# Kernel optimization log

Measured on AMD Instinct MI355X. Metric: run time of the kernel, lower is better.

Reference implementation:

```python
import jax, jax.numpy as jnp
import numpy as np
import math

B, T, C, H, L, V = 4, 2048, 256, 4, 2, 1024
HS = C // H  # head size


def setup_inputs() -> dict:
    key = jax.random.key(0)
    ks = jax.random.split(key, 10)
    s = 0.02
    return {
        "tokens": jax.random.randint(ks[0], (B, T), 0, V),
        "wte": s * jax.random.normal(ks[1], (V + 1, C), dtype=jnp.float32),
        "ln1_g": jnp.ones((L, C), jnp.float32),
        "ln1_b": jnp.zeros((L, C), jnp.float32),
        "attn_w": s * jax.random.normal(ks[2], (L, 3 * C, C), dtype=jnp.float32),
        "attn_b": jnp.zeros((L, 3 * C), jnp.float32),
        "proj_w": s * jax.random.normal(ks[3], (L, C, C), dtype=jnp.float32),
        "proj_b": jnp.zeros((L, C), jnp.float32),
        "embk": s * jax.random.normal(ks[4], (L, T, HS), dtype=jnp.float32),
        "embv": s * jax.random.normal(ks[5], (L, T, HS), dtype=jnp.float32),
        "ln2_g": jnp.ones((L, C), jnp.float32),
        "ln2_b": jnp.zeros((L, C), jnp.float32),
        "fc_w": s * jax.random.normal(ks[6], (L, 4 * C, C), dtype=jnp.float32),
        "fc_b": jnp.zeros((L, 4 * C), jnp.float32),
        "mproj_w": s * jax.random.normal(ks[7], (L, C, 4 * C), dtype=jnp.float32),
        "mproj_b": jnp.zeros((L, C), jnp.float32),
        "lnf_g": jnp.ones((C,), jnp.float32),
        "lnf_b": jnp.zeros((C,), jnp.float32),
        "head_w": s * jax.random.normal(ks[8], (V, C), dtype=jnp.float32),
    }


def _ln(x, g, b):
    mu = x.mean(-1, keepdims=True)
    var = x.var(-1, keepdims=True)
    return (x - mu) / jnp.sqrt(var + 1e-5) * g + b


def _gelu(x):  # NewGELU (tanh approximation)
    return 0.5 * x * (1.0 + jnp.tanh(math.sqrt(2.0 / math.pi) * (x + 0.044715 * x ** 3)))


def reference(tokens, wte, ln1_g, ln1_b, attn_w, attn_b, proj_w, proj_b,
              embk, embv, ln2_g, ln2_b, fc_w, fc_b, mproj_w, mproj_b,
              lnf_g, lnf_b, head_w):
    x = wte[tokens]  # [B,T,C]; no absolute pos emb in this model
    idx = jnp.arange(T)
    rel = jnp.tril(idx[:, None] - idx[None, :])  # [T,T] nonneg offsets
    causal = idx[:, None] >= idx[None, :]
    scale = 1.0 / math.sqrt(HS)
    for l in range(L):
        h = _ln(x, ln1_g[l], ln1_b[l])
        qkv = h @ attn_w[l].T + attn_b[l]  # [B,T,3C]
        q, k, v = jnp.split(qkv, 3, axis=-1)
        q = q.reshape(B, T, H, HS).transpose(0, 2, 1, 3)  # [B,H,T,hs]
        k = k.reshape(B, T, H, HS).transpose(0, 2, 1, 3)
        v = v.reshape(B, T, H, HS).transpose(0, 2, 1, 3)
        rk = embk[l][rel]  # [T,T,hs]
        rv = embv[l][rel]  # [T,T,hs]
        att = jnp.einsum('bhtd,bhsd->bhts', q, k) * scale \
            + jnp.einsum('bhtd,tsd->bhts', q, rk)
        att = jnp.where(causal, att, -jnp.inf)
        att = jax.nn.softmax(att, axis=-1)
        y = jnp.einsum('bhts,bhsd->bhtd', att, v) \
            + jnp.einsum('bhts,tsd->bhtd', att, rv)
        y = y.transpose(0, 2, 1, 3).reshape(B, T, C)
        x = x + (y @ proj_w[l].T + proj_b[l])
        h2 = _ln(x, ln2_g[l], ln2_b[l])
        x = x + (_gelu(h2 @ fc_w[l].T + fc_b[l]) @ mproj_w[l].T + mproj_b[l])
    x = _ln(x, lnf_g, lnf_b)
    return x @ head_w.T  # [B,T,V] logits
```

## Files before the change

### kernel.cpp

```cpp
#include <hip/hip_runtime.h>
#include <hip/hip_bf16.h>
#include <math.h>

#define BB 4
#define TT 2048
#define CC 256
#define HH 4
#define LL 2
#define VV 1024
#define HS 64
#define EPAD 2176
#define LOG2E 1.4426950408889634f

typedef __attribute__((ext_vector_type(8))) __bf16 bf16x8;
typedef __attribute__((ext_vector_type(4))) float f32x4;

#define MFMA16(a, b, c) __builtin_amdgcn_mfma_f32_16x16x32_bf16((a), (b), (c), 0, 0, 0)

__device__ __forceinline__ ushort f2bf(float f) {
    __hip_bfloat16 h = __float2bfloat16(f);
    return *reinterpret_cast<ushort*>(&h);
}
__device__ __forceinline__ float bf2f(ushort u) {
    union { uint i; float f; } c; c.i = ((uint)u) << 16; return c.f;
}

__device__ __forceinline__ void gload16(const void* g, void* l) {
    __builtin_amdgcn_global_load_lds(
        (const __attribute__((address_space(1))) void*)g,
        (__attribute__((address_space(3))) void*)l, 16, 0, 0);
}

__device__ __forceinline__ float gelu_f(float v) {
    return 0.5f * v * (1.0f + tanhf(0.7978845608028654f * (v + 0.044715f * v * v * v)));
}

__global__ void embed_kernel(const int* __restrict__ tok,
                             const float* __restrict__ wte,
                             float* __restrict__ x) {
    int row = blockIdx.x;
    int tid = threadIdx.x;
    int tk = tok[row];
    x[(size_t)row * CC + tid] = wte[(size_t)tk * CC + tid];
}

__global__ void cvt5_kernel(const float* __restrict__ w0, const float* __restrict__ w1,
                            const float* __restrict__ w2, const float* __restrict__ w3,
                            const float* __restrict__ w4,
                            ushort* __restrict__ o0, ushort* __restrict__ o1,
                            ushort* __restrict__ o2, ushort* __restrict__ o3,
                            ushort* __restrict__ o4) {
    int i = blockIdx.x * 256 + threadIdx.x;
    const float* src; ushort* dst; int j;
    if (i < 98304)       { src = w0; dst = o0; j = i; }
    else if (i < 131072) { src = w1; dst = o1; j = i - 98304; }
    else if (i < 262144) { src = w2; dst = o2; j = i - 131072; }
    else if (i < 393216) { src = w3; dst = o3; j = i - 262144; }
    else                 { src = w4; dst = o4; j = i - 393216; }
    float4 v = ((const float4*)src)[j];
    ushort4 o;
    o.x = f2bf(v.x); o.y = f2bf(v.y); o.z = f2bf(v.z); o.w = f2bf(v.w);
    ((ushort4*)dst)[j] = o;
}

__global__ __launch_bounds__(256) void ln_kernel(const float* __restrict__ x,
                                                 const float* __restrict__ g,
                                                 const float* __restrict__ b,
                                                 ushort* __restrict__ out) {
    int row = blockIdx.x * 4 + (threadIdx.x >> 6);
    int lane = threadIdx.x & 63;
    float4 v = ((const float4*)(x + (size_t)row * CC))[lane];
    float s = v.x + v.y + v.z + v.w;
    float s2 = v.x * v.x + v.y * v.y + v.z * v.z + v.w * v.w;
    for (int m = 1; m < 64; m <<= 1) {
        s += __shfl_xor(s, m);
        s2 += __shfl_xor(s2, m);
    }
    float mean = s * (1.0f / CC);
    float var = s2 * (1.0f / CC) - mean * mean;
    float rs = rsqrtf(var + 1e-5f);
    float4 gg = ((const float4*)g)[lane];
    float4 bb = ((const float4*)b)[lane];
    ushort4 o;
    o.x = f2bf((v.x - mean) * rs * gg.x + bb.x);
    o.y = f2bf((v.y - mean) * rs * gg.y + bb.y);
    o.z = f2bf((v.z - mean) * rs * gg.z + bb.z);
    o.w = f2bf((v.w - mean) * rs * gg.w + bb.w);
    ((ushort4*)(out + (size_t)row * CC))[lane] = o;
}

template<int MODE>
__global__ __launch_bounds__(256) void bgemm128_kernel(
        const ushort* __restrict__ A, const ushort* __restrict__ W,
        const float* __restrict__ bias, float* __restrict__ out,
        ushort* __restrict__ outb, int N, int K,
        ushort* __restrict__ qb, ushort* __restrict__ kb,
        ushort* __restrict__ vtb) {
    constexpr int ASUB = 8, TOT = 12, BUFSH = 192 * 32;
    __shared__ ushort lds[2 * BUFSH];
    int tid = threadIdx.x;
    int w = tid >> 6, lane = tid & 63;
    int lo = lane & 15, hi = lane >> 4;
    int row0 = blockIdx.y * 128;
    int col0 = blockIdx.x * 64;
    int wm = w >> 1, wn = w & 1;
    const ushort* Asrc = A + (size_t)row0 * K;
    const ushort* Wsrc = W + (size_t)col0 * K;

    auto STAGE = [&](int buf, int k0) {
        ushort* dst = &lds[buf * BUFSH];
        for (int s = w; s < TOT; s += 4) {
            const ushort* src;
            if (s < ASUB) src = Asrc + (size_t)(s * 16 + lo) * K + k0 + hi * 8;
            else          src = Wsrc + (size_t)((s - ASUB) * 16 + lo) * K + k0 + hi * 8;
            gload16(src, dst + s * 512);
        }
    };

    f32x4 acc[4][2] = {};
    int NT = K >> 5;
    STAGE(0, 0);
    asm volatile("s_waitcnt vmcnt(0)" ::: "memory");
    __syncthreads();
    for (int t = 0; t < NT; ++t) {
        int buf = t & 1;
        if (t + 1 < NT) STAGE(buf ^ 1, (t + 1) << 5);
        bf16x8 a[4], b[2];
#pragma unroll
        for (int f = 0; f < 4; ++f)
            a[f] = *(const bf16x8*)&lds[buf * BUFSH + (wm * 4 + f) * 512 + lane * 8];
#pragma unroll
        for (int g = 0; g < 2; ++g)
            b[g] = *(const bf16x8*)&lds[buf * BUFSH + (ASUB + wn * 2 + g) * 512 + lane * 8];
        __builtin_amdgcn_s_setprio(1);
#pragma unroll
        for (int f = 0; f < 4; ++f)
#pragma unroll
            for (int g = 0; g < 2; ++g)
                acc[f][g] = MFMA16(a[f], b[g], acc[f][g]);
        __builtin_amdgcn_s_setprio(0);
        asm volatile("s_waitcnt vmcnt(0)" ::: "memory");
        __syncthreads();
    }
#pragma unroll
    for (int f = 0; f < 4; ++f) {
        int rr = row0 + wm * 64 + f * 16 + hi * 4;
#pragma unroll
        for (int g = 0; g < 2; ++g) {
            int cc = col0 + wn * 32 + g * 16 + lo;
            float bv = bias ? bias[cc] : 0.0f;
#pragma unroll
            for (int j = 0; j < 4; ++j) {
                int r = rr + j;
                float v = acc[f][g][j] + bv;
                if (MODE == 3) {
                    int t = r & 2047, bb2 = r >> 11;
                    int which = cc >> 8, hh = (cc >> 6) & 3, dd = cc & 63;
                    size_t bh = (size_t)(bb2 * 4 + hh);
                    if (which == 0)      qb[(bh * 2048 + t) * 64 + dd] = f2bf(v);
                    else if (which == 1) kb[(bh * 2048 + t) * 64 + dd] = f2bf(v * (0.125f * LOG2E));
                    else                 vtb[(bh * 64 + dd) * 2048 + t] = f2bf(v);
                } else if (MODE == 2) {
                    outb[(size_t)r * N + cc] = f2bf(gelu_f(v));
                } else {
                    out[(size_t)r * N + cc] = v;
                }
            }
        }
    }
}

__global__ __launch_bounds__(256) void bgemm64_kernel(
        const ushort* __restrict__ A, const ushort* __restrict__ W,
        const float* __restrict__ bias, float* __restrict__ out,
        int N, int K) {
    constexpr int ASUB = 8, TOT = 16, BUFSH = 128 * 64;
    __shared__ ushort lds[2 * BUFSH];
    int tid = threadIdx.x;
    int w = tid >> 6, lane = tid & 63;
    int lo = lane & 15, hi = lane >> 4;
    int row0 = blockIdx.y * 64;
    int col0 = blockIdx.x * 64;
    const ushort* Asrc = A + (size_t)row0 * K;
    const ushort* Wsrc = W + (size_t)col0 * K;

    auto STAGE = [&](int buf, int k0) {
        ushort* dst = &lds[buf * BUFSH];
        for (int s = w; s < TOT; s += 4) {
            const ushort* src;
            if (s < ASUB) {
                int rg = s >> 1, kh = s & 1;
                src = Asrc + (size_t)(rg * 16 + lo) * K + k0 + kh * 32 + hi * 8;
            } else {
                int s2 = s - ASUB;
                int cg = s2 >> 1, kh = s2 & 1;
                src = Wsrc + (size_t)(cg * 16 + lo) * K + k0 + kh * 32 + hi * 8;
            }
            gload16(src, dst + s * 512);
        }
    };

    f32x4 acc[4] = {};
    int NT = K >> 6;
    STAGE(0, 0);
    asm volatile("s_waitcnt vmcnt(0)" ::: "memory");
    __syncthreads();
    for (int t = 0; t < NT; ++t) {
        int buf = t & 1;
        if (t + 1 < NT) STAGE(buf ^ 1, (t + 1) << 6);
        bf16x8 a[2];
#pragma unroll
        for (int kh = 0; kh < 2; ++kh)
            a[kh] = *(const bf16x8*)&lds[buf * BUFSH + (w * 2 + kh) * 512 + lane * 8];
        __builtin_amdgcn_s_setprio(1);
#pragma unroll
        for (int g = 0; g < 4; ++g) {
#pragma unroll
            for (int kh = 0; kh < 2; ++kh) {
                bf16x8 b = *(const bf16x8*)&lds[buf * BUFSH + (ASUB + g * 2 + kh) * 512 + lane * 8];
                acc[g] = MFMA16(a[kh], b, acc[g]);
            }
        }
        __builtin_amdgcn_s_setprio(0);
        asm volatile("s_waitcnt vmcnt(0)" ::: "memory");
        __syncthreads();
    }
#pragma unroll
    for (int g = 0; g < 4; ++g) {
        int cc = col0 + g * 16 + lo;
        float bv = bias ? bias[cc] : 0.0f;
#pragma unroll
        for (int j = 0; j < 4; ++j) {
            int r = row0 + w * 16 + hi * 4 + j;
            out[(size_t)r * N + cc] += acc[g][j] + bv;
        }
    }
}

__global__ void emb_bf_kernel(const float* __restrict__ ek,
                              const float* __restrict__ ev,
                              ushort* __restrict__ ekp,
                              ushort* __restrict__ evtp) {
    int i = blockIdx.x * 256 + threadIdx.x;
    int rp = i >> 6, d = i & 63;
    int o = rp - 64;
    bool in = (o >= 0 && o < TT);
    float kv = in ? ek[(size_t)o * 64 + d] * LOG2E : 0.0f;
    float vv = in ? ev[(size_t)o * 64 + d] : 0.0f;
    ekp[(size_t)rp * 64 + d] = f2bf(kv);
    evtp[(size_t)d * EPAD + rp] = f2bf(vv);
}

#define SBUF 57344
#define KOFF 0
#define VOFF 8192
#define EKOFF 16384
#define EVOFF 32768
#define WSCR (2 * SBUF)

__global__ __launch_bounds__(512, 2) void flash_kernel(
        const ushort* __restrict__ qb,
        const ushort* __restrict__ kb,
        const ushort* __restrict__ vtb,
        const ushort* __restrict__ ekp,
        const ushort* __restrict__ evtp,
        ushort* __restrict__ y) {
    extern __shared__ __align__(16) char dls[];

    int g = blockIdx.x;
    int lbid = ((g & 7) << 5) | (g >> 3);
    int bh = lbid >> 4;
    int pk = lbid & 15;
    int tid = threadIdx.x;
    int w = tid >> 6;
    int sub = w & 3;
    int h = w >> 2;
    int lane = tid & 63;
    int lo = lane & 15, hi = lane >> 4;
    int sw = (lo & 7) << 4;

    char* wbase = dls + WSCR + w * 6144;
    ushort (*Rl)[88]   = (ushort (*)[88])  wbase;
    ushort (*Pl)[72]   = (ushort (*)[72])  wbase;
    ushort (*Ppl)[104] = (ushort (*)[104])(wbase + 2816);

    {
        uint* pz = reinterpret_cast<uint*>(&Ppl[0][0]);
        for (int i = lane; i < 832; i += 64) pz[i] = 0;
    }

    const char* kB  = (const char*)(kb  + (size_t)bh * 2048 * 64);
    const char* vB  = (const char*)(vtb + (size_t)bh * 64 * 2048);
    const char* ekB = (const char*)ekp;
    const char* evB = (const char*)evtp;

    int t0A = (31 - pk) * 64, t0B = pk * 64;
    int NSA = 32 - pk;
    const int NC = 33;

    auto STAGE = [&](int buf, int ci) {
        int t0 = (ci < NSA) ? t0A : t0B;
        int s0 = ((ci < NSA) ? ci : ci - NSA) * 64;
        int band0 = t0 - s0;
        char* B = dls + buf * SBUF;
        int wb = (tid & 448) << 4;
        {
            int gb = tid * 16;
            int r = gb >> 7, c = gb & 127;
            gload16(kB + (size_t)(s0 + r) * 128 + (c ^ ((r & 7) << 4)), B + KOFF + wb);
        }
        {
            int gb = tid * 16;
            int r = gb >> 7, c = gb & 127;
            gload16(vB + (size_t)r * 4096 + (size_t)s0 * 2 + (c ^ ((r & 7) << 4)),
                    B + VOFF + wb);
        }
#pragma unroll
        for (int p = 0; p < 2; ++p) {
            int gb = p * 8192 + tid * 16;
            int r = gb >> 7, c = gb & 127;
            gload16(ekB + (size_t)(band0 + r) * 128 + (c ^ ((r & 7) << 4)),
                    B + EKOFF + p * 8192 + wb);
        }
#pragma unroll
        for (int p = 0; p < 3; ++p) {
            int gb = p * 8192 + tid * 16;
            int r = gb / 384, c = gb - r * 384;
            gload16(evB + (size_t)r * 4352 + (size_t)band0 * 2 + (c ^ ((r & 7) << 4)),
                    B + EVOFF + p * 8192 + wb);
        }
    };

    STAGE(0, 0);
    asm volatile("s_waitcnt vmcnt(0)" ::: "memory");
    __syncthreads();

    int b_ = bh >> 2, h_ = bh & 3;
    int buf = 0, ci = 0;
    int nb = h ? 0 : 2;
    int kcA = h ? 0 : 1, kcB = h ? 1 : 2;

    for (int tile = 0; tile < 2; ++tile) {
        int t0 = tile ? t0B : t0A;
        int NS = tile ? (pk + 1) : NSA;

        const ushort* qbase = qb + ((size_t)bh * 2048 + t0 + sub * 16) * 64;
        bf16x8 qf0 = *(const bf16x8*)(qbase + (size_t)lo * 64 + hi * 8);
        bf16x8 qf1 = *(const bf16x8*)(qbase + (size_t)lo * 64 + 32 + hi * 8);

        float rs[4] = {0.0f, 0.0f, 0.0f, 0.0f};
        f32x4 O[4] = {};

        for (int c = 0; c < NS; ++c, ++ci) {
            if (ci + 1 < NC) STAGE(buf ^ 1, ci + 1);
            const char* B = dls + buf * SBUF;
            bool diag = (c == NS - 1);

            f32x4 sacc[2] = {};
            __builtin_amdgcn_s_setprio(1);
#pragma unroll
            for (int ni = 0; ni < 2; ++ni) {
                int R = (2 * h + ni) * 16 + lo;
                bf16x8 b0 = *(const bf16x8*)(B + KOFF + R * 128 + ((hi * 16) ^ sw));
                bf16x8 b1 = *(const bf16x8*)(B + KOFF + R * 128 + ((64 + hi * 16) ^ sw));
                sacc[ni] = MFMA16(qf0, b0, sacc[ni]);
                sacc[ni] = MFMA16(qf1, b1, sacc[ni]);
            }
#pragma unroll
            for (int ni = 0; ni < 3; ++ni) {
                int n = nb + ni;
                int RL = (sub + n) * 16 + lo;
                f32x4 r = {};
                bf16x8 e0 = *(const bf16x8*)(B + EKOFF + RL * 128 + ((hi * 16) ^ sw));
                bf16x8 e1 = *(const bf16x8*)(B + EKOFF + RL * 128 + ((64 + hi * 16) ^ sw));
                r = MFMA16(qf0, e0, r);
                r = MFMA16(qf1, e1, r);
#pragma unroll
                for (int j = 0; j < 4; ++j) Rl[hi * 4 + j][n * 16 + lo] = f2bf(r[j]);
            }
            __builtin_amdgcn_s_setprio(0);
            float sv[2][4];
#pragma unroll
            for (int ni = 0; ni < 2; ++ni) {
                int sl = (2 * h + ni) * 16 + lo;
#pragma unroll
                for (int j = 0; j < 4; ++j) {
                    int r_ = hi * 4 + j;
                    sv[ni][j] = sacc[ni][j] + bf2f(Rl[r_][r_ - sl + 64]);
                }
            }
            asm volatile("" ::: "memory");
#pragma unroll
            for (int ni = 0; ni < 2; ++ni) {
                int sl = (2 * h + ni) * 16 + lo;
#pragma unroll
                for (int j = 0; j < 4; ++j) {
                    int r_ = hi * 4 + j;
                    float p = (!diag || sl <= sub * 16 + r_) ? exp2f(sv[ni][j]) : 0.0f;
                    rs[j] += p;
                    ushort pu = f2bf(p);
                    Pl[r_][sl] = pu;
                    Ppl[r_][r_ - sl + 64] = pu;
                }
            }
            asm volatile("" ::: "memory");

            __builtin_amdgcn_s_setprio(1);
            bf16x8 pa  = *(const bf16x8*)(&Pl[lo][h * 32 + hi * 8]);
            bf16x8 pb0 = *(const bf16x8*)(&Ppl[lo][kcA * 32 + hi * 8]);
            bf16x8 pb1 = *(const bf16x8*)(&Ppl[lo][kcB * 32 + hi * 8]);
#pragma unroll
            for (int n = 0; n < 4; ++n) {
                int R = n * 16 + lo;
                bf16x8 bv = *(const bf16x8*)(B + VOFF + R * 128 + ((h * 64 + hi * 16) ^ sw));
                O[n] = MFMA16(pa, bv, O[n]);
                bf16x8 e0 = *(const bf16x8*)(B + EVOFF + R * 384 +
                                             ((sub * 32 + kcA * 64 + hi * 16) ^ sw));
                O[n] = MFMA16(pb0, e0, O[n]);
                bf16x8 e1 = *(const bf16x8*)(B + EVOFF + R * 384 +
                                             ((sub * 32 + kcB * 64 + hi * 16) ^ sw));
                O[n] = MFMA16(pb1, e1, O[n]);
            }
            __builtin_amdgcn_s_setprio(0);
            asm volatile("" ::: "memory");

            asm volatile("s_waitcnt vmcnt(0)" ::: "memory");
            __syncthreads();
            buf ^= 1;
        }

#pragma unroll
        for (int msk = 1; msk < 16; msk <<= 1)
#pragma unroll
            for (int j = 0; j < 4; ++j) rs[j] += __shfl_xor(rs[j], msk);

        char* mscr = dls + (buf ^ 1) * SBUF + sub * 8192;
        if (h == 1) {
            float* Of = (float*)mscr;
#pragma unroll
            for (int n = 0; n < 4; ++n)
#pragma unroll
                for (int j = 0; j < 4; ++j)
                    Of[(hi * 4 + j) * 64 + n * 16 + lo] = O[n][j];
            if (lo == 0)
#pragma unroll
                for (int j = 0; j < 4; ++j)
                    ((float*)(mscr + 4096))[hi * 4 + j] = rs[j];
        }
        __syncthreads();
        if (h == 0) {
            float* Of = (float*)mscr;
            float inv[4];
#pragma unroll
            for (int j = 0; j < 4; ++j)
                inv[j] = 1.0f / (rs[j] + ((float*)(mscr + 4096))[hi * 4 + j]);
#pragma unroll
            for (int n = 0; n < 4; ++n)
#pragma unroll
                for (int j = 0; j < 4; ++j) {
                    int r = t0 + sub * 16 + hi * 4 + j;
                    float v = O[n][j] + Of[(hi * 4 + j) * 64 + n * 16 + lo];
                    y[((size_t)(b_ * 2048 + r)) * 256 + h_ * 64 + n * 16 + lo] =
                        f2bf(v * inv[j]);
                }
        }
        __syncthreads();
    }
}

extern "C" void kernel_launch(void* const* d_in, const int* in_sizes, int n_in,
                              void* d_out, int out_size, void* d_ws, size_t ws_size,
                              hipStream_t stream) {
    const int*   tokens  = (const int*)d_in[0];
    const float* wte     = (const float*)d_in[1];
    const float* ln1_g   = (const float*)d_in[2];
    const float* ln1_b   = (const float*)d_in[3];
    const float* attn_w  = (const float*)d_in[4];
    const float* attn_b  = (const float*)d_in[5];
    const float* proj_w  = (const float*)d_in[6];
    const float* proj_b  = (const float*)d_in[7];
    const float* embk    = (const float*)d_in[8];
    const float* embv    = (const float*)d_in[9];
    const float* ln2_g   = (const float*)d_in[10];
    const float* ln2_b   = (const float*)d_in[11];
    const float* fc_w    = (const float*)d_in[12];
    const float* fc_b    = (const float*)d_in[13];
    const float* mproj_w = (const float*)d_in[14];
    const float* mproj_b = (const float*)d_in[15];
    const float* lnf_g   = (const float*)d_in[16];
    const float* lnf_b   = (const float*)d_in[17];
    const float* head_w  = (const float*)d_in[18];
    float* out = (float*)d_out;

    const int M = BB * TT;
    char* wsb = (char*)d_ws;
    float*  x    = (float*)wsb;
    ushort* h    = (ushort*)(wsb + ((size_t)8 << 20));
    ushort* y    = (ushort*)(wsb + ((size_t)12 << 20));
    ushort* qb   = (ushort*)(wsb + ((size_t)16 << 20));
    ushort* kbf  = (ushort*)(wsb + ((size_t)20 << 20));
    ushort* vtb  = (ushort*)(wsb + ((size_t)24 << 20));
    ushort* ekp  = (ushort*)(wsb + ((size_t)28 << 20));
    ushort* evtp = (ushort*)(wsb + ((size_t)28 << 20) + 524288);
    ushort* attn_wb  = (ushort*)(wsb + ((size_t)29 << 20));
    ushort* proj_wb  = attn_wb + (size_t)LL * 3 * CC * CC;
    ushort* fc_wb    = proj_wb + (size_t)LL * CC * CC;
    ushort* mproj_wb = fc_wb + (size_t)LL * 4 * CC * CC;
    ushort* head_wb  = mproj_wb + (size_t)LL * CC * 4 * CC;
    ushort* fcb = (ushort*)d_out;

    dim3 blk(256);
    const int FLDS = WSCR + 8 * 6144;
    hipFuncSetAttribute(reinterpret_cast<const void*>(flash_kernel),
                        hipFuncAttributeMaxDynamicSharedMemorySize, FLDS);

    cvt5_kernel<<<dim3(1792), blk, 0, stream>>>(
        attn_w, proj_w, fc_w, mproj_w, head_w,
        attn_wb, proj_wb, fc_wb, mproj_wb, head_wb);

    embed_kernel<<<dim3(M), blk, 0, stream>>>(tokens, wte, x);

    for (int l = 0; l < LL; l++) {
        ln_kernel<<<dim3(M / 4), blk, 0, stream>>>(x, ln1_g + l * CC, ln1_b + l * CC, h);
        bgemm128_kernel<3><<<dim3(12, 64), blk, 0, stream>>>(
            h, attn_wb + (size_t)l * 3 * CC * CC, attn_b + (size_t)l * 3 * CC,
            nullptr, nullptr, 3 * CC, CC, qb, kbf, vtb);
        emb_bf_kernel<<<dim3(EPAD * 64 / 256), blk, 0, stream>>>(
            embk + (size_t)l * TT * HS, embv + (size_t)l * TT * HS, ekp, evtp);
        flash_kernel<<<dim3(256), dim3(512), FLDS, stream>>>(qb, kbf, vtb, ekp, evtp, y);
        bgemm64_kernel<<<dim3(4, 128), blk, 0, stream>>>(
            y, proj_wb + (size_t)l * CC * CC, proj_b + (size_t)l * CC,
            x, CC, CC);
        ln_kernel<<<dim3(M / 4), blk, 0, stream>>>(x, ln2_g + l * CC, ln2_b + l * CC, h);
        bgemm128_kernel<2><<<dim3(16, 64), blk, 0, stream>>>(
            h, fc_wb + (size_t)l * 4 * CC * CC, fc_b + (size_t)l * 4 * CC,
            nullptr, fcb, 4 * CC, CC, nullptr, nullptr, nullptr);
        bgemm64_kernel<<<dim3(4, 128), blk, 0, stream>>>(
            fcb, mproj_wb + (size_t)l * CC * 4 * CC, mproj_b + (size_t)l * CC,
            x, CC, 4 * CC);
    }

    ln_kernel<<<dim3(M / 4), blk, 0, stream>>>(x, lnf_g, lnf_b, h);
    bgemm128_kernel<0><<<dim3(16, 64), blk, 0, stream>>>(
        h, head_wb, nullptr, out, nullptr, VV, CC, nullptr, nullptr, nullptr);
}
```

Baseline: 335.5 us.

## Load full K=256 tiles into LDS once and widen K=1024 GEMM tiles

For the K=256 GEMMs, the new kernel loads the whole 128x256 A tile and 64x256 W tile into dynamic LDS in a single burst. It then runs eight MFMA k-steps with no per-step barrier or double buffering. The proj and mproj GEMMs (previously 64-row tiles, K chunks of 64) now use 128x64 tiles with K chunks of 128 and a 4x2 accumulator per warp. The aim is to cut barriers and raise reuse per load, at the cost of 96KB LDS per block, which lowers occupancy, and halved grid sizes for the N=256 GEMMs.

```diff
diff --git a/kernel.cpp b/kernel.cpp
--- a/kernel.cpp
+++ b/kernel.cpp
@@ -90,58 +90,55 @@
 }
 
 template<int MODE>
-__global__ __launch_bounds__(256) void bgemm128_kernel(
+__global__ __launch_bounds__(256) void bgfull_kernel(
         const ushort* __restrict__ A, const ushort* __restrict__ W,
         const float* __restrict__ bias, float* __restrict__ out,
-        ushort* __restrict__ outb, int N, int K,
+        ushort* __restrict__ outb, int N,
         ushort* __restrict__ qb, ushort* __restrict__ kb,
         ushort* __restrict__ vtb) {
-    constexpr int ASUB = 8, TOT = 12, BUFSH = 192 * 32;
-    __shared__ ushort lds[2 * BUFSH];
+    extern __shared__ ushort flds[];
+    const int K = 256;
     int tid = threadIdx.x;
     int w = tid >> 6, lane = tid & 63;
     int lo = lane & 15, hi = lane >> 4;
     int row0 = blockIdx.y * 128;
     int col0 = blockIdx.x * 64;
     int wm = w >> 1, wn = w & 1;
-    const ushort* Asrc = A + (size_t)row0 * K;
-    const ushort* Wsrc = W + (size_t)col0 * K;
-
-    auto STAGE = [&](int buf, int k0) {
-        ushort* dst = &lds[buf * BUFSH];
-        for (int s = w; s < TOT; s += 4) {
-            const ushort* src;
-            if (s < ASUB) src = Asrc + (size_t)(s * 16 + lo) * K + k0 + hi * 8;
-            else          src = Wsrc + (size_t)((s - ASUB) * 16 + lo) * K + k0 + hi * 8;
-            gload16(src, dst + s * 512);
-        }
-    };
-
-    f32x4 acc[4][2] = {};
-    int NT = K >> 5;
-    STAGE(0, 0);
+
+#pragma unroll
+    for (int i = 0; i < 24; ++i) {
+        int s = w * 24 + i;
+        if (s < 64) {
+            int rg = s >> 3, kg = s & 7;
+            gload16(A + (size_t)(row0 + rg * 16 + lo) * K + kg * 32 + hi * 8,
+                    &flds[s * 512]);
+        } else {
+            int s2 = s - 64;
+            int cg = s2 >> 3, kg = s2 & 7;
+            gload16(W + (size_t)(col0 + cg * 16 + lo) * K + kg * 32 + hi * 8,
+                    &flds[32768 + s2 * 512]);
+        }
+    }
     asm volatile("s_waitcnt vmcnt(0)" ::: "memory");
     __syncthreads();
-    for (int t = 0; t < NT; ++t) {
-        int buf = t & 1;
-        if (t + 1 < NT) STAGE(buf ^ 1, (t + 1) << 5);
+
+    f32x4 acc[4][2] = {};
+#pragma unroll
+    for (int kg = 0; kg < 8; ++kg) {
         bf16x8 a[4], b[2];
 #pragma unroll
         for (int f = 0; f < 4; ++f)
-            a[f] = *(const bf16x8*)&lds[buf * BUFSH + (wm * 4 + f) * 512 + lane * 8];
+            a[f] = *(const bf16x8*)&flds[((wm * 4 + f) * 8 + kg) * 512 + lane * 8];
 #pragma unroll
         for (int g = 0; g < 2; ++g)
-            b[g] = *(const bf16x8*)&lds[buf * BUFSH + (ASUB + wn * 2 + g) * 512 + lane * 8];
-        __builtin_amdgcn_s_setprio(1);
+            b[g] = *(const bf16x8*)&flds[32768 + ((wn * 2 + g) * 8 + kg) * 512 + lane * 8];
 #pragma unroll
         for (int f = 0; f < 4; ++f)
 #pragma unroll
             for (int g = 0; g < 2; ++g)
                 acc[f][g] = MFMA16(a[f], b[g], acc[f][g]);
-        __builtin_amdgcn_s_setprio(0);
-        asm volatile("s_waitcnt vmcnt(0)" ::: "memory");
-        __syncthreads();
-    }
+    }
+
 #pragma unroll
     for (int f = 0; f < 4; ++f) {
         int rr = row0 + wm * 64 + f * 16 + hi * 4;
@@ -162,6 +159,8 @@
                     else                 vtb[(bh * 64 + dd) * 2048 + t] = f2bf(v);
                 } else if (MODE == 2) {
                     outb[(size_t)r * N + cc] = f2bf(gelu_f(v));
+                } else if (MODE == 1) {
+                    out[(size_t)r * N + cc] += v;
                 } else {
                     out[(size_t)r * N + cc] = v;
                 }
@@ -170,69 +169,71 @@
     }
 }
 
-__global__ __launch_bounds__(256) void bgemm64_kernel(
+__global__ __launch_bounds__(256) void bgk1024_kernel(
         const ushort* __restrict__ A, const ushort* __restrict__ W,
-        const float* __restrict__ bias, float* __restrict__ out,
-        int N, int K) {
-    constexpr int ASUB = 8, TOT = 16, BUFSH = 128 * 64;
-    __shared__ ushort lds[2 * BUFSH];
+        const float* __restrict__ bias, float* __restrict__ out, int N) {
+    extern __shared__ ushort flds[];
+    const int K = 1024;
+    constexpr int BUF = 24576;
     int tid = threadIdx.x;
     int w = tid >> 6, lane = tid & 63;
     int lo = lane & 15, hi = lane >> 4;
-    int row0 = blockIdx.y * 64;
+    int row0 = blockIdx.y * 128;
     int col0 = blockIdx.x * 64;
-    const ushort* Asrc = A + (size_t)row0 * K;
-    const ushort* Wsrc = W + (size_t)col0 * K;
+    int wm = w >> 1, wn = w & 1;
 
     auto STAGE = [&](int buf, int k0) {
-        ushort* dst = &lds[buf * BUFSH];
-        for (int s = w; s < TOT; s += 4) {
-            const ushort* src;
-            if (s < ASUB) {
-                int rg = s >> 1, kh = s & 1;
-                src = Asrc + (size_t)(rg * 16 + lo) * K + k0 + kh * 32 + hi * 8;
+#pragma unroll
+        for (int i = 0; i < 12; ++i) {
+            int s = w * 12 + i;
+            if (s < 32) {
+                int rg = s >> 2, kg = s & 3;
+                gload16(A + (size_t)(row0 + rg * 16 + lo) * K + k0 + kg * 32 + hi * 8,
+                        &flds[buf * BUF + s * 512]);
             } else {
-                int s2 = s - ASUB;
-                int cg = s2 >> 1, kh = s2 & 1;
-                src = Wsrc + (size_t)(cg * 16 + lo) * K + k0 + kh * 32 + hi * 8;
-            }
-            gload16(src, dst + s * 512);
+                int s2 = s - 32;
+                int cg = s2 >> 2, kg = s2 & 3;
+                gload16(W + (size_t)(col0 + cg * 16 + lo) * K + k0 + kg * 32 + hi * 8,
+                        &flds[buf * BUF + 16384 + s2 * 512]);
+            }
         }
     };
 
-    f32x4 acc[4] = {};
-    int NT = K >> 6;
+    f32x4 acc[4][2] = {};
     STAGE(0, 0);
     asm volatile("s_waitcnt vmcnt(0)" ::: "memory");
     __syncthreads();
-    for (int t = 0; t < NT; ++t) {
+    for (int t = 0; t < 8; ++t) {
         int buf = t & 1;
-        if (t + 1 < NT) STAGE(buf ^ 1, (t + 1) << 6);
-        bf16x8 a[2];
-#pragma unroll
-        for (int kh = 0; kh < 2; ++kh)
-            a[kh] = *(const bf16x8*)&lds[buf * BUFSH + (w * 2 + kh) * 512 + lane * 8];
-        __builtin_amdgcn_s_setprio(1);
-#pragma unroll
-        for (int g = 0; g < 4; ++g) {
-#pragma unroll
-            for (int kh = 0; kh < 2; ++kh) {
-                bf16x8 b = *(const bf16x8*)&lds[buf * BUFSH + (ASUB + g * 2 + kh) * 512 + lane * 8];
-                acc[g] = MFMA16(a[kh], b, acc[g]);
-            }
-        }
-        __builtin_amdgcn_s_setprio(0);
+        if (t + 1 < 8) STAGE(buf ^ 1, (t + 1) * 128);
+#pragma unroll
+        for (int kg = 0; kg < 4; ++kg) {
+            bf16x8 a[4], b[2];
+#pragma unroll
+            for (int f = 0; f < 4; ++f)
+                a[f] = *(const bf16x8*)&flds[buf * BUF + ((wm * 4 + f) * 4 + kg) * 512 + lane * 8];
+#pragma unroll
+            for (int g = 0; g < 2; ++g)
+                b[g] = *(const bf16x8*)&flds[buf * BUF + 16384 + ((wn * 2 + g) * 4 + kg) * 512 + lane * 8];
+#pragma unroll
+            for (int f = 0; f < 4; ++f)
+#pragma unroll
+                for (int g = 0; g < 2; ++g)
+                    acc[f][g] = MFMA16(a[f], b[g], acc[f][g]);
+        }
         asm volatile("s_waitcnt vmcnt(0)" ::: "memory");
         __syncthreads();
     }
 #pragma unroll
-    for (int g = 0; g < 4; ++g) {
-        int cc = col0 + g * 16 + lo;
-        float bv = bias ? bias[cc] : 0.0f;
-#pragma unroll
-        for (int j = 0; j < 4; ++j) {
-            int r = row0 + w * 16 + hi * 4 + j;
-            out[(size_t)r * N + cc] += acc[g][j] + bv;
+    for (int f = 0; f < 4; ++f) {
+        int rr = row0 + wm * 64 + f * 16 + hi * 4;
+#pragma unroll
+        for (int g = 0; g < 2; ++g) {
+            int cc = col0 + wn * 32 + g * 16 + lo;
+            float bv = bias ? bias[cc] : 0.0f;
+#pragma unroll
+            for (int j = 0; j < 4; ++j)
+                out[(size_t)(rr + j) * N + cc] += acc[f][g][j] + bv;
         }
     }
 }
@@ -511,8 +512,19 @@
 
     dim3 blk(256);
     const int FLDS = WSCR + 8 * 6144;
+    const int GLDS = 98304;
     hipFuncSetAttribute(reinterpret_cast<const void*>(flash_kernel),
                         hipFuncAttributeMaxDynamicSharedMemorySize, FLDS);
+    hipFuncSetAttribute(reinterpret_cast<const void*>(bgfull_kernel<0>),
+                        hipFuncAttributeMaxDynamicSharedMemorySize, GLDS);
+    hipFuncSetAttribute(reinterpret_cast<const void*>(bgfull_kernel<1>),
+                        hipFuncAttributeMaxDynamicSharedMemorySize, GLDS);
+    hipFuncSetAttribute(reinterpret_cast<const void*>(bgfull_kernel<2>),
+                        hipFuncAttributeMaxDynamicSharedMemorySize, GLDS);
+    hipFuncSetAttribute(reinterpret_cast<const void*>(bgfull_kernel<3>),
+                        hipFuncAttributeMaxDynamicSharedMemorySize, GLDS);
+    hipFuncSetAttribute(reinterpret_cast<const void*>(bgk1024_kernel),
+                        hipFuncAttributeMaxDynamicSharedMemorySize, GLDS);
 
     cvt5_kernel<<<dim3(1792), blk, 0, stream>>>(
         attn_w, proj_w, fc_w, mproj_w, head_w,
@@ -522,25 +534,25 @@
 
     for (int l = 0; l < LL; l++) {
         ln_kernel<<<dim3(M / 4), blk, 0, stream>>>(x, ln1_g + l * CC, ln1_b + l * CC, h);
-        bgemm128_kernel<3><<<dim3(12, 64), blk, 0, stream>>>(
+        bgfull_kernel<3><<<dim3(12, 64), blk, GLDS, stream>>>(
             h, attn_wb + (size_t)l * 3 * CC * CC, attn_b + (size_t)l * 3 * CC,
-            nullptr, nullptr, 3 * CC, CC, qb, kbf, vtb);
+            nullptr, nullptr, 3 * CC, qb, kbf, vtb);
         emb_bf_kernel<<<dim3(EPAD * 64 / 256), blk, 0, stream>>>(
             embk + (size_t)l * TT * HS, embv + (size_t)l * TT * HS, ekp, evtp);
         flash_kernel<<<dim3(256), dim3(512), FLDS, stream>>>(qb, kbf, vtb, ekp, evtp, y);
-        bgemm64_kernel<<<dim3(4, 128), blk, 0, stream>>>(
+        bgfull_kernel<1><<<dim3(4, 64), blk, GLDS, stream>>>(
             y, proj_wb + (size_t)l * CC * CC, proj_b + (size_t)l * CC,
-            x, CC, CC);
+            x, nullptr, CC, nullptr, nullptr, nullptr);
         ln_kernel<<<dim3(M / 4), blk, 0, stream>>>(x, ln2_g + l * CC, ln2_b + l * CC, h);
-        bgemm128_kernel<2><<<dim3(16, 64), blk, 0, stream>>>(
+        bgfull_kernel<2><<<dim3(16, 64), blk, GLDS, stream>>>(
             h, fc_wb + (size_t)l * 4 * CC * CC, fc_b + (size_t)l * 4 * CC,
-            nullptr, fcb, 4 * CC, CC, nullptr, nullptr, nullptr);
-        bgemm64_kernel<<<dim3(4, 128), blk, 0, stream>>>(
+            nullptr, fcb, 4 * CC, nullptr, nullptr, nullptr);
+        bgk1024_kernel<<<dim3(4, 64), blk, GLDS, stream>>>(
             fcb, mproj_wb + (size_t)l * CC * 4 * CC, mproj_b + (size_t)l * CC,
-            x, CC, 4 * CC);
+            x, CC);
     }
 
     ln_kernel<<<dim3(M / 4), blk, 0, stream>>>(x, lnf_g, lnf_b, h);
-    bgemm128_kernel<0><<<dim3(16, 64), blk, 0, stream>>>(
-        h, head_wb, nullptr, out, nullptr, VV, CC, nullptr, nullptr, nullptr);
-}
+    bgfull_kernel<0><<<dim3(16, 64), blk, GLDS, stream>>>(
+        h, head_wb, nullptr, out, nullptr, VV, nullptr, nullptr, nullptr);
+}
```

Measured after the change: 399.9 us. 1.19x slower.

## Widen bf16 GEMM tiles to 128x128 with 512 threads; hoist rel-emb conversion

Applied to the files above, without the earlier changes.

The 128-row GEMM kernel now uses 512-thread blocks covering 128x128 output tiles instead of 128x64, so each staged A tile is reused across twice as many columns and the grid has half as many blocks. The relative-position embedding bf16 conversion for both layers is done once up front in a single launch rather than once per layer. The wider tile halves the block count for the QKV, FC and head GEMMs, which may lower occupancy and load balance on this many CUs. The epilogue indexing appears to carry over the old column layout unchanged, which may need checking.

```diff
diff --git a/kernel.cpp b/kernel.cpp
--- a/kernel.cpp
+++ b/kernel.cpp
@@ -90,31 +90,27 @@
 }
 
 template<int MODE>
-__global__ __launch_bounds__(256) void bgemm128_kernel(
+__global__ __launch_bounds__(512) void bgemm256_kernel(
         const ushort* __restrict__ A, const ushort* __restrict__ W,
         const float* __restrict__ bias, float* __restrict__ out,
         ushort* __restrict__ outb, int N, int K,
         ushort* __restrict__ qb, ushort* __restrict__ kb,
         ushort* __restrict__ vtb) {
-    constexpr int ASUB = 8, TOT = 12, BUFSH = 192 * 32;
+    constexpr int BUFSH = 16 * 512;
     __shared__ ushort lds[2 * BUFSH];
     int tid = threadIdx.x;
     int w = tid >> 6, lane = tid & 63;
     int lo = lane & 15, hi = lane >> 4;
     int row0 = blockIdx.y * 128;
-    int col0 = blockIdx.x * 64;
-    int wm = w >> 1, wn = w & 1;
+    int col0 = blockIdx.x * 128;
+    int wm = w >> 2, wn = w & 3;
     const ushort* Asrc = A + (size_t)row0 * K;
     const ushort* Wsrc = W + (size_t)col0 * K;
 
     auto STAGE = [&](int buf, int k0) {
         ushort* dst = &lds[buf * BUFSH];
-        for (int s = w; s < TOT; s += 4) {
-            const ushort* src;
-            if (s < ASUB) src = Asrc + (size_t)(s * 16 + lo) * K + k0 + hi * 8;
-            else          src = Wsrc + (size_t)((s - ASUB) * 16 + lo) * K + k0 + hi * 8;
-            gload16(src, dst + s * 512);
-        }
+        gload16(Asrc + (size_t)(w * 16 + lo) * K + k0 + hi * 8, dst + w * 512);
+        gload16(Wsrc + (size_t)(w * 16 + lo) * K + k0 + hi * 8, dst + (8 + w) * 512);
     };
 
     f32x4 acc[4][2] = {};
@@ -131,7 +127,7 @@
             a[f] = *(const bf16x8*)&lds[buf * BUFSH + (wm * 4 + f) * 512 + lane * 8];
 #pragma unroll
         for (int g = 0; g < 2; ++g)
-            b[g] = *(const bf16x8*)&lds[buf * BUFSH + (ASUB + wn * 2 + g) * 512 + lane * 8];
+            b[g] = *(const bf16x8*)&lds[buf * BUFSH + (8 + wn * 2 + g) * 512 + lane * 8];
         __builtin_amdgcn_s_setprio(1);
 #pragma unroll
         for (int f = 0; f < 4; ++f)
@@ -237,18 +233,20 @@
     }
 }
 
-__global__ void emb_bf_kernel(const float* __restrict__ ek,
-                              const float* __restrict__ ev,
-                              ushort* __restrict__ ekp,
-                              ushort* __restrict__ evtp) {
+__global__ void emb_bf2_kernel(const float* __restrict__ ek,
+                               const float* __restrict__ ev,
+                               ushort* __restrict__ ekp,
+                               ushort* __restrict__ evtp) {
     int i = blockIdx.x * 256 + threadIdx.x;
-    int rp = i >> 6, d = i & 63;
+    int l = i / (EPAD * 64);
+    int j = i - l * (EPAD * 64);
+    int rp = j >> 6, d = j & 63;
     int o = rp - 64;
     bool in = (o >= 0 && o < TT);
-    float kv = in ? ek[(size_t)o * 64 + d] * LOG2E : 0.0f;
-    float vv = in ? ev[(size_t)o * 64 + d] : 0.0f;
-    ekp[(size_t)rp * 64 + d] = f2bf(kv);
-    evtp[(size_t)d * EPAD + rp] = f2bf(vv);
+    float kv = in ? ek[(size_t)l * TT * HS + (size_t)o * 64 + d] * LOG2E : 0.0f;
+    float vv = in ? ev[(size_t)l * TT * HS + (size_t)o * 64 + d] : 0.0f;
+    ekp[(size_t)l * EPAD * 64 + (size_t)rp * 64 + d] = f2bf(kv);
+    evtp[(size_t)l * 64 * EPAD + (size_t)d * EPAD + rp] = f2bf(vv);
 }
 
 #define SBUF 57344
@@ -501,8 +499,8 @@
     ushort* kbf  = (ushort*)(wsb + ((size_t)20 << 20));
     ushort* vtb  = (ushort*)(wsb + ((size_t)24 << 20));
     ushort* ekp  = (ushort*)(wsb + ((size_t)28 << 20));
-    ushort* evtp = (ushort*)(wsb + ((size_t)28 << 20) + 524288);
-    ushort* attn_wb  = (ushort*)(wsb + ((size_t)29 << 20));
+    ushort* evtp = ekp + (size_t)LL * EPAD * 64;
+    ushort* attn_wb  = (ushort*)(wsb + ((size_t)30 << 20));
     ushort* proj_wb  = attn_wb + (size_t)LL * 3 * CC * CC;
     ushort* fc_wb    = proj_wb + (size_t)LL * CC * CC;
     ushort* mproj_wb = fc_wb + (size_t)LL * 4 * CC * CC;
@@ -517,22 +515,22 @@
     cvt5_kernel<<<dim3(1792), blk, 0, stream>>>(
         attn_w, proj_w, fc_w, mproj_w, head_w,
         attn_wb, proj_wb, fc_wb, mproj_wb, head_wb);
-
+    emb_bf2_kernel<<<dim3(LL * EPAD * 64 / 256), blk, 0, stream>>>(
+        embk, embv, ekp, evtp);
     embed_kernel<<<dim3(M), blk, 0, stream>>>(tokens, wte, x);
 
     for (int l = 0; l < LL; l++) {
         ln_kernel<<<dim3(M / 4), blk, 0, stream>>>(x, ln1_g + l * CC, ln1_b + l * CC, h);
-        bgemm128_kernel<3><<<dim3(12, 64), blk, 0, stream>>>(
+        bgemm256_kernel<3><<<dim3(6, 64), dim3(512), 0, stream>>>(
             h, attn_wb + (size_t)l * 3 * CC * CC, attn_b + (size_t)l * 3 * CC,
             nullptr, nullptr, 3 * CC, CC, qb, kbf, vtb);
-        emb_bf_kernel<<<dim3(EPAD * 64 / 256), blk, 0, stream>>>(
-            embk + (size_t)l * TT * HS, embv + (size_t)l * TT * HS, ekp, evtp);
-        flash_kernel<<<dim3(256), dim3(512), FLDS, stream>>>(qb, kbf, vtb, ekp, evtp, y);
+        flash_kernel<<<dim3(256), dim3(512), FLDS, stream>>>(
+            qb, kbf, vtb, ekp + (size_t)l * EPAD * 64, evtp + (size_t)l * 64 * EPAD, y);
         bgemm64_kernel<<<dim3(4, 128), blk, 0, stream>>>(
             y, proj_wb + (size_t)l * CC * CC, proj_b + (size_t)l * CC,
             x, CC, CC);
         ln_kernel<<<dim3(M / 4), blk, 0, stream>>>(x, ln2_g + l * CC, ln2_b + l * CC, h);
-        bgemm128_kernel<2><<<dim3(16, 64), blk, 0, stream>>>(
+        bgemm256_kernel<2><<<dim3(8, 64), dim3(512), 0, stream>>>(
             h, fc_wb + (size_t)l * 4 * CC * CC, fc_b + (size_t)l * 4 * CC,
             nullptr, fcb, 4 * CC, CC, nullptr, nullptr, nullptr);
         bgemm64_kernel<<<dim3(4, 128), blk, 0, stream>>>(
@@ -541,6 +539,6 @@
     }
 
     ln_kernel<<<dim3(M / 4), blk, 0, stream>>>(x, lnf_g, lnf_b, h);
-    bgemm128_kernel<0><<<dim3(16, 64), blk, 0, stream>>>(
+    bgemm256_kernel<0><<<dim3(8, 64), dim3(512), 0, stream>>>(
         h, head_wb, nullptr, out, nullptr, VV, CC, nullptr, nullptr, nullptr);
 }
```

New measurement: 331.0 us. No clear change (-1.3%).
